# Kernel optimization log

Measured on AMD Instinct MI355X. Metric: run time of the kernel, lower is better.

Reference implementation:

```python
import jax, jax.numpy as jnp
import numpy as np

GROUP_SIZE = 8
REQUIRED_ZEROS = 4


def _dorefa_quantize(x, bits):
    # tanh-normalize-round
    t = jnp.tanh(x).astype(jnp.float32)
    y = t / jnp.max(jnp.abs(t))
    delta = float(2 ** (bits - 1) - 1)
    _y = jnp.round(y * delta)

    out_c, in_c, h, w = _y.shape
    if in_c < GROUP_SIZE:
        return _y / delta

    g = in_c // GROUP_SIZE
    keep = GROUP_SIZE - REQUIRED_ZEROS  # keep at most 4 non-zeros per group

    # [out_c, g*8, h, w] -> [out_c, g, h, w, 8] (group axis last for top_k)
    yg = _y[:, : g * GROUP_SIZE].reshape(out_c, g, GROUP_SIZE, h, w)
    yg = jnp.transpose(yg, (0, 1, 3, 4, 2))

    # The torch loop zeroes the smallest-|v| non-zeros until >=4 zeros per
    # group. Equivalently: keep only the `keep` largest-|v| entries of each
    # group (zeros have |v|=0, so groups already having >=4 zeros are
    # unchanged). Fully vectorized via batched top-k + one-hot mask.
    absv = jnp.abs(yg)
    _, idx = jax.lax.top_k(absv, keep)                      # [o,g,h,w,keep]
    mask = jax.nn.one_hot(idx, GROUP_SIZE, dtype=yg.dtype).sum(axis=-2)
    yg = yg * mask                                          # [o,g,h,w,8]

    yg = jnp.transpose(yg, (0, 1, 4, 2, 3)).reshape(out_c, g * GROUP_SIZE, h, w)
    out = jnp.concatenate([yg, _y[:, g * GROUP_SIZE :]], axis=1) if g * GROUP_SIZE < in_c else yg
    return out / delta


def setup_inputs() -> dict:
    key = jax.random.key(0)
    x = jax.random.normal(key, (2048, 2048, 3, 3), dtype=jnp.float32)
    return {"x": x, "bits": 8}


def reference(x, bits):
    return _dorefa_quantize(x, bits)
```

## Files before the change

kernel.cpp:

```cpp
#include <hip/hip_runtime.h>
#include <math.h>

#define HW        9
#define GROUP     8
#define KEEP      4
#define DELTA     127.0f
#define INV_DELTA (1.0f / 127.0f)
#define GB_FLOATS 72

#define GB_TILE   32
#define TILE_F    (GB_TILE * GB_FLOATS)
#define TILE_CH   (TILE_F / 256)
#define CELLS     (GB_TILE * HW)
#define WPB       4

typedef float f32x4 __attribute__((ext_vector_type(4)));

__global__ void maxabs_kernel(const float4* __restrict__ x, unsigned* __restrict__ ws, int n4) {
    __shared__ float red[4];
    float m = 0.0f;
    int stride = gridDim.x * blockDim.x;
    #pragma unroll 4
    for (int i = blockIdx.x * blockDim.x + threadIdx.x; i < n4; i += stride) {
        float4 v = x[i];
        m = fmaxf(m, fmaxf(fmaxf(fabsf(v.x), fabsf(v.y)),
                           fmaxf(fabsf(v.z), fabsf(v.w))));
    }
    #pragma unroll
    for (int off = 32; off > 0; off >>= 1)
        m = fmaxf(m, __shfl_down(m, off, 64));
    int wave = threadIdx.x >> 6;
    if ((threadIdx.x & 63) == 0) red[wave] = m;
    __syncthreads();
    if (threadIdx.x == 0) {
        float b = fmaxf(fmaxf(red[0], red[1]), fmaxf(red[2], red[3]));
        atomicMax(ws, __float_as_uint(b));
    }
}

__device__ __attribute__((noinline)) float ref_rz(float xx, float M) {
    float td = (float)tanh((double)xx);
    float y  = td / M;
    return rintf(y * DELTA);
}

__device__ __forceinline__ float fast_tanh(float x) {
    float ax  = fabsf(x);
    float axc = fminf(ax, 10.0f);
    float E   = __expf(2.0f * axc);
    float num = E - 1.0f;
    float den = E + 1.0f;
    float r0  = __builtin_amdgcn_rcpf(den);
    float r   = r0 * fmaf(-den, r0, 2.0f);
    float tl  = copysignf(num * r, x);
    float s = x * x;
    float p = fmaf(s, 0.0035921280f, -0.0088632358f);
    p = fmaf(s, p, 0.021869488f);
    p = fmaf(s, p, -0.053968254f);
    p = fmaf(s, p, 0.13333334f);
    p = fmaf(s, p, -0.33333334f);
    float ts = fmaf(x * s, p, x);
    return (ax <= 0.5f) ? ts : tl;
}

__global__ __launch_bounds__(256, 4) void quant_kernel(const float* __restrict__ x,
                             float* __restrict__ out,
                             const unsigned* __restrict__ ws,
                             int n_gb) {
    __shared__ float lds[WPB][TILE_F];
    __shared__ float sM, sC;
    if (threadIdx.x == 0) {
        float mm = (float)tanh((double)__uint_as_float(*ws));
        sM = mm;
        sC = (float)(127.0 / (double)mm);
    }
    __syncthreads();
    float M = sM, C = sC;

    const int wv   = threadIdx.x >> 6;
    const int lane = threadIdx.x & 63;
    const int tile = blockIdx.x * WPB + wv;
    if (tile * GB_TILE >= n_gb) return;

    const size_t base = (size_t)tile * TILE_F;
    const float* src  = x + base;
    float* ldsw       = &lds[wv][0];

    #pragma unroll
    for (int k = 0; k < TILE_CH; ++k) {
        __builtin_amdgcn_global_load_lds(
            (__attribute__((address_space(1))) void*)(src + k * 256 + lane * 4),
            (__attribute__((address_space(3))) void*)(ldsw + k * 256),
            16, 0, 0);
    }
    asm volatile("s_waitcnt vmcnt(0)" ::: "memory");
    __builtin_amdgcn_sched_barrier(0);

    for (int c = 0; c < (CELLS + 63) / 64; ++c) {
        int ci = lane + 64 * c;
        if (ci < CELLS) {
            int gb = ci / 9;
            int hw = ci - gb * 9;
            float* cell = ldsw + gb * GB_FLOATS + hw;

            float v8[GROUP], a8[GROUP];
            #pragma unroll
            for (int j = 0; j < GROUP; ++j) {
                float xx = cell[9 * j];
                float t  = fast_tanh(xx);
                float z  = t * C;
                float rz = rintf(z);
                float d  = 0.5f - fabsf(z - rz);
                if (d < fmaf(2e-6f, fabsf(z), 5e-7f))
                    rz = ref_rz(xx, M);
                v8[j] = rz;
                a8[j] = fabsf(rz);
            }
            int rank[GROUP] = {0, 0, 0, 0, 0, 0, 0, 0};
            #pragma unroll
            for (int i = 0; i < GROUP; ++i) {
                #pragma unroll
                for (int j = i + 1; j < GROUP; ++j) {
                    bool ge = (a8[i] >= a8[j]);
                    rank[j] += ge ? 1 : 0;
                    rank[i] += ge ? 0 : 1;
                }
            }
            #pragma unroll
            for (int j = 0; j < GROUP; ++j)
                cell[9 * j] = (rank[j] < KEEP) ? (v8[j] * INV_DELTA) : 0.0f;
        }
    }
    __builtin_amdgcn_sched_barrier(0);

    f32x4* dst4       = (f32x4*)(out + base);
    const f32x4* l4   = (const f32x4*)ldsw;
    #pragma unroll
    for (int k = 0; k < TILE_CH; ++k) {
        __builtin_nontemporal_store(l4[k * 64 + lane], &dst4[k * 64 + lane]);
    }
}

extern "C" void kernel_launch(void* const* d_in, const int* in_sizes, int n_in,
                              void* d_out, int out_size, void* d_ws, size_t ws_size,
                              hipStream_t stream) {
    const float* x = (const float*)d_in[0];
    float* out = (float*)d_out;
    unsigned* ws = (unsigned*)d_ws;

    int n = in_sizes[0];
    int n4 = n / 4;
    int n_gb = n / GB_FLOATS;

    hipMemsetAsync(ws, 0, sizeof(unsigned), stream);

    maxabs_kernel<<<2048, 256, 0, stream>>>((const float4*)x, ws, n4);

    int blocks_q = (n_gb + GB_TILE * WPB - 1) / (GB_TILE * WPB);
    quant_kernel<<<blocks_q, 256, 0, stream>>>(x, out, ws, n_gb);
}
```

Measured before the change: 295.0 us.

## Double-buffer LDS tiles per wave to overlap global loads with compute

Each wave now processes eight consecutive tiles with two LDS buffers. The next tile's global-to-LDS loads are issued while the current tile is computed and stored, with explicit vmcnt waits sequencing the pipeline. This is meant to hide memory latency that the one-tile-per-wave version exposed. In exchange, LDS use doubles and the occupancy hint drops to 2. The grid size now assumes the group-block count divides evenly, so there is no tail handling.

Result: slower. 319.0 us (+8.1%).

```diff
diff --git a/kernel.cpp b/kernel.cpp
--- a/kernel.cpp
+++ b/kernel.cpp
@@ -13,8 +13,14 @@
 #define TILE_CH   (TILE_F / 256)
 #define CELLS     (GB_TILE * HW)
 #define WPB       4
+#define NT        8
 
 typedef float f32x4 __attribute__((ext_vector_type(4)));
+
+template <int N>
+__device__ __forceinline__ void wait_vmcnt() {
+    asm volatile("s_waitcnt vmcnt(%0)" :: "n"(N) : "memory");
+}
 
 __global__ void maxabs_kernel(const float4* __restrict__ x, unsigned* __restrict__ ws, int n4) {
     __shared__ float red[4];
@@ -63,39 +69,8 @@
     return (ax <= 0.5f) ? ts : tl;
 }
 
-__global__ __launch_bounds__(256, 4) void quant_kernel(const float* __restrict__ x,
-                             float* __restrict__ out,
-                             const unsigned* __restrict__ ws,
-                             int n_gb) {
-    __shared__ float lds[WPB][TILE_F];
-    __shared__ float sM, sC;
-    if (threadIdx.x == 0) {
-        float mm = (float)tanh((double)__uint_as_float(*ws));
-        sM = mm;
-        sC = (float)(127.0 / (double)mm);
-    }
-    __syncthreads();
-    float M = sM, C = sC;
-
-    const int wv   = threadIdx.x >> 6;
-    const int lane = threadIdx.x & 63;
-    const int tile = blockIdx.x * WPB + wv;
-    if (tile * GB_TILE >= n_gb) return;
-
-    const size_t base = (size_t)tile * TILE_F;
-    const float* src  = x + base;
-    float* ldsw       = &lds[wv][0];
-
+__device__ __forceinline__ void compute_tile(float* ldsw, int lane, float M, float C) {
     #pragma unroll
-    for (int k = 0; k < TILE_CH; ++k) {
-        __builtin_amdgcn_global_load_lds(
-            (__attribute__((address_space(1))) void*)(src + k * 256 + lane * 4),
-            (__attribute__((address_space(3))) void*)(ldsw + k * 256),
-            16, 0, 0);
-    }
-    asm volatile("s_waitcnt vmcnt(0)" ::: "memory");
-    __builtin_amdgcn_sched_barrier(0);
-
     for (int c = 0; c < (CELLS + 63) / 64; ++c) {
         int ci = lane + 64 * c;
         if (ci < CELLS) {
@@ -131,13 +106,74 @@
                 cell[9 * j] = (rank[j] < KEEP) ? (v8[j] * INV_DELTA) : 0.0f;
         }
     }
-    __builtin_amdgcn_sched_barrier(0);
+}
 
-    f32x4* dst4       = (f32x4*)(out + base);
-    const f32x4* l4   = (const f32x4*)ldsw;
+__global__ __launch_bounds__(256, 2) void quant_kernel(const float* __restrict__ x,
+                             float* __restrict__ out,
+                             const unsigned* __restrict__ ws,
+                             int n_gb) {
+    __shared__ float lds[WPB][2][TILE_F];
+    __shared__ float sM, sC;
+    if (threadIdx.x == 0) {
+        float mm = (float)tanh((double)__uint_as_float(*ws));
+        sM = mm;
+        sC = (float)(127.0 / (double)mm);
+    }
+    __syncthreads();
+    float M = sM, C = sC;
+
+    const int wv   = threadIdx.x >> 6;
+    const int lane = threadIdx.x & 63;
+    const int wave_id = blockIdx.x * WPB + wv;
+
+    const size_t tbase0 = (size_t)wave_id * NT * TILE_F;
+
     #pragma unroll
-    for (int k = 0; k < TILE_CH; ++k) {
-        __builtin_nontemporal_store(l4[k * 64 + lane], &dst4[k * 64 + lane]);
+    for (int b = 0; b < 2; ++b) {
+        const float* src = x + tbase0 + (size_t)b * TILE_F;
+        float* ldsw = &lds[wv][b][0];
+        #pragma unroll
+        for (int k = 0; k < TILE_CH; ++k) {
+            __builtin_amdgcn_global_load_lds(
+                (__attribute__((address_space(1))) void*)(src + k * 256 + lane * 4),
+                (__attribute__((address_space(3))) void*)(ldsw + k * 256),
+                16, 0, 0);
+        }
+    }
+
+    #pragma unroll
+    for (int i = 0; i < NT; ++i) {
+        if (i == 0)            wait_vmcnt<9>();
+        else if (i == 1)       wait_vmcnt<18>();
+        else if (i == NT - 1)  wait_vmcnt<18>();
+        else                   wait_vmcnt<27>();
+        __builtin_amdgcn_sched_barrier(0);
+
+        float* ldsw = &lds[wv][i & 1][0];
+        compute_tile(ldsw, lane, M, C);
+
+        f32x4 sv[TILE_CH];
+        const f32x4* l4 = (const f32x4*)ldsw;
+        #pragma unroll
+        for (int k = 0; k < TILE_CH; ++k) sv[k] = l4[k * 64 + lane];
+        asm volatile("s_waitcnt lgkmcnt(0)" ::: "memory");
+        __builtin_amdgcn_sched_barrier(0);
+
+        if (i + 2 < NT) {
+            const float* src = x + tbase0 + (size_t)(i + 2) * TILE_F;
+            #pragma unroll
+            for (int k = 0; k < TILE_CH; ++k) {
+                __builtin_amdgcn_global_load_lds(
+                    (__attribute__((address_space(1))) void*)(src + k * 256 + lane * 4),
+                    (__attribute__((address_space(3))) void*)(ldsw + k * 256),
+                    16, 0, 0);
+            }
+        }
+
+        f32x4* dst4 = (f32x4*)(out + tbase0 + (size_t)i * TILE_F);
+        #pragma unroll
+        for (int k = 0; k < TILE_CH; ++k)
+            __builtin_nontemporal_store(sv[k], &dst4[k * 64 + lane]);
     }
 }
 
@@ -156,6 +192,6 @@
 
     maxabs_kernel<<<2048, 256, 0, stream>>>((const float4*)x, ws, n4);
 
-    int blocks_q = (n_gb + GB_TILE * WPB - 1) / (GB_TILE * WPB);
+    int blocks_q = n_gb / (GB_TILE * NT * WPB);
     quant_kernel<<<blocks_q, 256, 0, stream>>>(x, out, ws, n_gb);
 }
```
